# Kernel optimization log

Measured on AMD Instinct MI355X. Metric: run time of the kernel, lower is better.

Reference implementation:

```python
import jax, jax.numpy as jnp
import numpy as np

HEADS = 8
DIM_HEAD = 32
TOP_K = 256
KMEANS_ITERS = 10
EPS_LN = 1e-6
EPS_L2 = 1e-12


def chan_layer_norm(x, gamma, beta):
    # x: (b, c, L); normalize across channel dim (biased variance)
    mean = jnp.mean(x, axis=1, keepdims=True)
    var = jnp.var(x, axis=1, keepdims=True)
    return gamma * (x - mean) / (jnp.sqrt(var) + EPS_LN) + beta


def l2norm_ch(t):
    # F.normalize(t, dim=1): L2-normalize over channel axis of (B, c, L)
    n = jnp.linalg.norm(t, axis=1, keepdims=True)
    return t / jnp.maximum(n, EPS_L2)


def conv1x1(x, w):
    # x: (b, c_in, L), w: (c_out, c_in)  -> (b, c_out, L)
    return jnp.einsum('oc,bcl->bol', w, x)


def _dist2(x, c):
    # squared L2 distances, x: (N, d), c: (k, d) -> (N, k)
    return (jnp.sum(x * x, -1, keepdims=True)
            - 2.0 * x @ c.T
            + jnp.sum(c * c, -1)[None, :])


def kmeans_fit(x, k, iters):
    # Lloyd's algorithm, deterministic init = first k points
    c0 = x[:k]

    def step(c, _):
        assign = jnp.argmin(_dist2(x, c), axis=-1)           # (N,)
        sums = jax.ops.segment_sum(x, assign, num_segments=k)
        cnts = jax.ops.segment_sum(jnp.ones((x.shape[0],), x.dtype), assign,
                                   num_segments=k)
        new_c = jnp.where(cnts[:, None] > 0,
                          sums / jnp.maximum(cnts, 1.0)[:, None], c)
        return new_c, None

    c, _ = jax.lax.scan(step, c0, None, length=iters)
    return c


def select_best_ind(q, k, v, top_k):
    # q: (B, Lq, d), k/v: (B, Lk, d); B = b*heads
    B, Lk, d = k.shape
    q_flat = q.reshape(-1, d)
    centroids = kmeans_fit(q_flat, top_k, KMEANS_ITERS)       # (top_k, d)
    k_flat = k.reshape(-1, d)
    k_cluster = jnp.argmin(_dist2(k_flat, centroids), axis=-1).reshape(B, Lk)
    k_centers = centroids[k_cluster]                          # (B, Lk, d)
    k_dist = jnp.sum(jnp.abs(k_centers - k), axis=-1)         # (B, Lk)
    _, best_k = jax.lax.top_k(k_dist, top_k)                  # largest dists
    idx = best_k[:, :, None]
    k_sel = jnp.take_along_axis(k, idx, axis=1)
    v_sel = jnp.take_along_axis(v, idx, axis=1)
    return k_sel, v_sel


def reference(query_source, context, w_q, w_kv, w_out,
              ln_ctx_gamma, ln_ctx_beta, ln_q_gamma, ln_q_beta,
              ln_out_gamma, ln_out_beta, gamma_scale):
    b, c, L_query = query_source.shape
    ctx = chan_layer_norm(context, ln_ctx_gamma, ln_ctx_beta)
    qs = chan_layer_norm(query_source, ln_q_gamma, ln_q_beta)

    kv = conv1x1(ctx, w_kv)                                   # (b, 2*inner, Lc)
    k, v = jnp.split(kv, 2, axis=1)
    q = conv1x1(qs, w_q)                                      # (b, inner, Lq)

    def fold(t):  # b (h c) L -> (b h) c L
        B, hc, L = t.shape
        return t.reshape(B, HEADS, DIM_HEAD, L).reshape(B * HEADS, DIM_HEAD, L)

    q, k, v = fold(q), fold(k), fold(v)
    q, k = l2norm_ch(q), l2norm_ch(k)
    # b d L -> b L d
    q = jnp.swapaxes(q, 1, 2)
    k = jnp.swapaxes(k, 1, 2)
    v = jnp.swapaxes(v, 1, 2)

    k, v = select_best_ind(q, k, v, TOP_K)

    sim = jnp.einsum('bid,bjd->bij', q, k)                    # (b*h, Lq, top_k)
    attn = jax.nn.softmax(sim, axis=-1)
    out = jnp.einsum('bij,bjd->bid', attn, v)                 # (b*h, Lq, dh)

    out = out.reshape(b, HEADS, L_query, DIM_HEAD)
    out = jnp.transpose(out, (0, 1, 3, 2)).reshape(b, HEADS * DIM_HEAD, L_query)
    out = conv1x1(out, w_out)
    out = chan_layer_norm(out, ln_out_gamma, ln_out_beta)
    return gamma_scale[0] * out + query_source


def setup_inputs() -> dict:
    key = jax.random.key(0)
    ks = jax.random.split(key, 8)
    dim, inner = 256, HEADS * DIM_HEAD
    b, Lq, Lc = 2, 4096, 4096
    inp = {
        'query_source': jax.random.normal(ks[0], (b, dim, Lq), jnp.float32),
        'context': jax.random.normal(ks[1], (b, dim, Lc), jnp.float32),
        'w_q': jax.random.normal(ks[2], (inner, dim), jnp.float32) * 0.05,
        'w_kv': jax.random.normal(ks[3], (2 * inner, dim), jnp.float32) * 0.05,
        'w_out': jax.random.normal(ks[4], (dim, inner), jnp.float32) * 0.05,
        'ln_ctx_gamma': jnp.ones((1, dim, 1), jnp.float32),
        'ln_ctx_beta': jnp.zeros((1, dim, 1), jnp.float32),
        'ln_q_gamma': jnp.ones((1, dim, 1), jnp.float32),
        'ln_q_beta': jnp.zeros((1, dim, 1), jnp.float32),
        'ln_out_gamma': jnp.ones((1, dim, 1), jnp.float32),
        'ln_out_beta': jnp.zeros((1, dim, 1), jnp.float32),
        'gamma_scale': jax.random.normal(ks[5], (1,), jnp.float32),
    }
    return inp
```

## Files before the change

### kernel.cpp

```cpp
#include <hip/hip_runtime.h>
#include <math.h>

#define CDIM 256
#define LSEQ 4096
#define NBH 16
#define NPTS 65536
#define KC 256

__device__ __forceinline__ float fadd(float a, float b){ return __fadd_rn(a,b); }
__device__ __forceinline__ float fmul(float a, float b){ return __fmul_rn(a,b); }
__device__ __forceinline__ float fsub(float a, float b){ return __fsub_rn(a,b); }

__device__ __forceinline__ float sum32_np(const float* e){
    float l[16];
    #pragma unroll
    for (int j = 0; j < 16; j++) l[j] = fadd(e[j], e[j + 16]);
    float t3[8];
    #pragma unroll
    for (int j = 0; j < 8; j++) t3[j] = fadd(l[j], l[j + 8]);
    float t6[4];
    #pragma unroll
    for (int j = 0; j < 4; j++) t6[j] = fadd(t3[j], t3[j + 4]);
    return fadd(fadd(t6[0], t6[2]), fadd(t6[1], t6[3]));
}

__global__ __launch_bounds__(64) void ln2_np(
        const float* __restrict__ x0, const float* __restrict__ g0,
        const float* __restrict__ bt0, float* __restrict__ y0,
        const float* __restrict__ x1, const float* __restrict__ g1,
        const float* __restrict__ bt1, float* __restrict__ y1) {
    int gid = blockIdx.x * 64 + threadIdx.x;
    int which = gid >> 13;
    int r = gid & 8191;
    int b = r >> 12, l = r & 4095;
    const float* x  = which ? x1 : x0;
    const float* g  = which ? g1 : g0;
    const float* bt = which ? bt1 : bt0;
    float* y        = which ? y1 : y0;
    const float* xb = x + (size_t)b * CDIM * LSEQ + l;
    float s = 0.f;
    #pragma unroll 8
    for (int c = 0; c < 256; c++) s = fadd(s, xb[(size_t)c * LSEQ]);
    float mean = __fdiv_rn(s, 256.f);
    float s2 = 0.f;
    #pragma unroll 8
    for (int c = 0; c < 256; c++) {
        float d = fsub(xb[(size_t)c * LSEQ], mean);
        s2 = fadd(s2, fmul(d, d));
    }
    float var = __fdiv_rn(s2, 256.f);
    float den = fadd(__fsqrt_rn(var), 1e-6f);
    float* yb = y + (size_t)b * CDIM * LSEQ + l;
    #pragma unroll 4
    for (int c = 0; c < 256; c++) {
        float d = fsub(xb[(size_t)c * LSEQ], mean);
        yb[(size_t)c * LSEQ] = fadd(__fdiv_rn(fmul(g[c], d), den), bt[c]);
    }
}

__global__ __launch_bounds__(256) void conv_all(
        const float* __restrict__ Wkv, const float* __restrict__ Xkv,
        float* __restrict__ Ykv,
        const float* __restrict__ Wq, const float* __restrict__ Xq,
        float* __restrict__ Yq) {
    __shared__ float ws[8 * 256];
    int tid = threadIdx.x;
    int l0 = blockIdx.x * 512 + tid * 2;
    bool qpath = blockIdx.y >= 64;
    int yb = qpath ? (blockIdx.y - 64) : blockIdx.y;
    int o0 = yb * 8;
    int b = blockIdx.z;
    const float* W = qpath ? Wq : Wkv;
    const float* X = qpath ? Xq : Xkv;
    {
        const float4* wb4 = (const float4*)(W + (size_t)o0 * CDIM);
        float4* ws4s = (float4*)ws;
        for (int i = tid; i < 8 * 64; i += 256) ws4s[i] = wb4[i];
    }
    __syncthreads();
    const float* xb = X + (size_t)b * CDIM * LSEQ;
    float acc[8][2];
    #pragma unroll
    for (int oo = 0; oo < 8; oo++) { acc[oo][0] = 0.f; acc[oo][1] = 0.f; }
    const float4* ws4 = (const float4*)ws;
    bool sop = qpath || (blockIdx.y < 32);
    if (sop) {
        for (int c = 0; c < 256; c += 4) {
            float2 x0q = *(const float2*)(xb + (size_t)(c + 0) * LSEQ + l0);
            float2 x1q = *(const float2*)(xb + (size_t)(c + 1) * LSEQ + l0);
            float2 x2q = *(const float2*)(xb + (size_t)(c + 2) * LSEQ + l0);
            float2 x3q = *(const float2*)(xb + (size_t)(c + 3) * LSEQ + l0);
            #pragma unroll
            for (int oo = 0; oo < 8; oo++) {
                float4 w = ws4[(oo * 256 + c) >> 2];
                acc[oo][0] = fadd(acc[oo][0], fmul(w.x, x0q.x));
                acc[oo][0] = fadd(acc[oo][0], fmul(w.y, x1q.x));
                acc[oo][0] = fadd(acc[oo][0], fmul(w.z, x2q.x));
                acc[oo][0] = fadd(acc[oo][0], fmul(w.w, x3q.x));
                acc[oo][1] = fadd(acc[oo][1], fmul(w.x, x0q.y));
                acc[oo][1] = fadd(acc[oo][1], fmul(w.y, x1q.y));
                acc[oo][1] = fadd(acc[oo][1], fmul(w.z, x2q.y));
                acc[oo][1] = fadd(acc[oo][1], fmul(w.w, x3q.y));
            }
        }
    } else {
        for (int c = 0; c < 256; c += 4) {
            float2 x0q = *(const float2*)(xb + (size_t)(c + 0) * LSEQ + l0);
            float2 x1q = *(const float2*)(xb + (size_t)(c + 1) * LSEQ + l0);
            float2 x2q = *(const float2*)(xb + (size_t)(c + 2) * LSEQ + l0);
            float2 x3q = *(const float2*)(xb + (size_t)(c + 3) * LSEQ + l0);
            #pragma unroll
            for (int oo = 0; oo < 8; oo++) {
                float4 w = ws4[(oo * 256 + c) >> 2];
                acc[oo][0] = __builtin_fmaf(w.x, x0q.x, acc[oo][0]);
                acc[oo][0] = __builtin_fmaf(w.y, x1q.x, acc[oo][0]);
                acc[oo][0] = __builtin_fmaf(w.z, x2q.x, acc[oo][0]);
                acc[oo][0] = __builtin_fmaf(w.w, x3q.x, acc[oo][0]);
                acc[oo][1] = __builtin_fmaf(w.x, x0q.y, acc[oo][1]);
                acc[oo][1] = __builtin_fmaf(w.y, x1q.y, acc[oo][1]);
                acc[oo][1] = __builtin_fmaf(w.z, x2q.y, acc[oo][1]);
                acc[oo][1] = __builtin_fmaf(w.w, x3q.y, acc[oo][1]);
            }
        }
    }
    float* Y = qpath ? Yq : Ykv;
    int rows = qpath ? 256 : 512;
    #pragma unroll
    for (int oo = 0; oo < 8; oo++)
        *(float2*)(Y + ((size_t)b * rows + o0 + oo) * LSEQ + l0) =
            make_float2(acc[oo][0], acc[oo][1]);
}

template<bool EXACT>
__global__ __launch_bounds__(256) void conv_q8(const float* __restrict__ W,
        const float* __restrict__ X, float* __restrict__ Y) {
    __shared__ float ws[8 * 256];
    int tid = threadIdx.x;
    int l0 = blockIdx.x * 512 + tid * 2;
    int o0 = blockIdx.y * 8;
    int b = blockIdx.z;
    {
        const float4* wb4 = (const float4*)(W + (size_t)o0 * CDIM);
        float4* ws4s = (float4*)ws;
        for (int i = tid; i < 8 * 64; i += 256) ws4s[i] = wb4[i];
    }
    __syncthreads();
    const float* xb = X + (size_t)b * CDIM * LSEQ;
    float acc[8][2];
    #pragma unroll
    for (int oo = 0; oo < 8; oo++) { acc[oo][0] = 0.f; acc[oo][1] = 0.f; }
    const float4* ws4 = (const float4*)ws;
    for (int c = 0; c < 256; c += 4) {
        float2 x0q = *(const float2*)(xb + (size_t)(c + 0) * LSEQ + l0);
        float2 x1q = *(const float2*)(xb + (size_t)(c + 1) * LSEQ + l0);
        float2 x2q = *(const float2*)(xb + (size_t)(c + 2) * LSEQ + l0);
        float2 x3q = *(const float2*)(xb + (size_t)(c + 3) * LSEQ + l0);
        #pragma unroll
        for (int oo = 0; oo < 8; oo++) {
            float4 w = ws4[(oo * 256 + c) >> 2];
            if (EXACT) {
                acc[oo][0] = fadd(acc[oo][0], fmul(w.x, x0q.x));
                acc[oo][0] = fadd(acc[oo][0], fmul(w.y, x1q.x));
                acc[oo][0] = fadd(acc[oo][0], fmul(w.z, x2q.x));
                acc[oo][0] = fadd(acc[oo][0], fmul(w.w, x3q.x));
                acc[oo][1] = fadd(acc[oo][1], fmul(w.x, x0q.y));
                acc[oo][1] = fadd(acc[oo][1], fmul(w.y, x1q.y));
                acc[oo][1] = fadd(acc[oo][1], fmul(w.z, x2q.y));
                acc[oo][1] = fadd(acc[oo][1], fmul(w.w, x3q.y));
            } else {
                acc[oo][0] = __builtin_fmaf(w.x, x0q.x, acc[oo][0]);
                acc[oo][0] = __builtin_fmaf(w.y, x1q.x, acc[oo][0]);
                acc[oo][0] = __builtin_fmaf(w.z, x2q.x, acc[oo][0]);
                acc[oo][0] = __builtin_fmaf(w.w, x3q.x, acc[oo][0]);
                acc[oo][1] = __builtin_fmaf(w.x, x0q.y, acc[oo][1]);
                acc[oo][1] = __builtin_fmaf(w.y, x1q.y, acc[oo][1]);
                acc[oo][1] = __builtin_fmaf(w.z, x2q.y, acc[oo][1]);
                acc[oo][1] = __builtin_fmaf(w.w, x3q.y, acc[oo][1]);
            }
        }
    }
    #pragma unroll
    for (int oo = 0; oo < 8; oo++)
        *(float2*)(Y + ((size_t)b * 256 + o0 + oo) * LSEQ + l0) =
            make_float2(acc[oo][0], acc[oo][1]);
}

__device__ __forceinline__ void fold_body(const float* __restrict__ src,
        int srcRows, int row0, int donorm, float* __restrict__ dst,
        float* __restrict__ xxout, float* __restrict__ centout,
        float* __restrict__ ccout, int p) {
    int bh = p >> 12, l = p & 4095;
    int b = bh >> 3, h = bh & 7;
    const float* sp = src + ((size_t)b * srcRows + row0 + h * 32) * LSEQ + l;
    float x[32];
    #pragma unroll
    for (int t = 0; t < 32; t++) x[t] = sp[(size_t)t * LSEQ];
    float4* dp4 = (float4*)(dst + (size_t)p * 32);
    if (donorm) {
        float ss = 0.f;
        #pragma unroll
        for (int t = 0; t < 32; t++) ss = fadd(ss, fmul(x[t], x[t]));
        float n = __fsqrt_rn(ss);
        float den = fmaxf(n, 1e-12f);
        #pragma unroll
        for (int t = 0; t < 32; t++) x[t] = __fdiv_rn(x[t], den);
    }
    #pragma unroll
    for (int t = 0; t < 8; t++)
        dp4[t] = make_float4(x[4*t], x[4*t+1], x[4*t+2], x[4*t+3]);
    if (xxout) {
        float e[32];
        #pragma unroll
        for (int t = 0; t < 32; t++) e[t] = fmul(x[t], x[t]);
        float xv = sum32_np(e);
        xxout[p] = xv;
        if (centout && p < KC) {
            float4* cp4 = (float4*)(centout + (size_t)p * 32);
            #pragma unroll
            for (int t = 0; t < 8; t++)
                cp4[t] = make_float4(x[4*t], x[4*t+1], x[4*t+2], x[4*t+3]);
            ccout[p] = xv;
        }
    }
}

__global__ __launch_bounds__(256) void fold3_np(const float* __restrict__ kvbuf,
        const float* __restrict__ qbuf, float* __restrict__ k_t,
        float* __restrict__ v_t, float* __restrict__ q_t,
        float* __restrict__ xx, float* __restrict__ cent, float* __restrict__ cc) {
    int blk = blockIdx.x, tid = threadIdx.x;
    if (blk < 256) {
        fold_body(kvbuf, 512, 0, 1, k_t, nullptr, nullptr, nullptr, blk * 256 + tid);
    } else if (blk < 512) {
        fold_body(kvbuf, 512, 256, 0, v_t, nullptr, nullptr, nullptr, (blk - 256) * 256 + tid);
    } else {
        fold_body(qbuf, 256, 0, 1, q_t, xx, cent, cc, (blk - 512) * 256 + tid);
    }
}

__global__ __launch_bounds__(512, 2) void assign4p(const float* __restrict__ pts,
        const float* __restrict__ xx, const float* __restrict__ cent,
        const float* __restrict__ cc, int* __restrict__ asn, int* __restrict__ hist) {
    __shared__ float sc[8192];
    __shared__ float scc[256];
    __shared__ int bins[256];
    int tid = threadIdx.x, c = blockIdx.x;
    {
        const float4* c4 = (const float4*)cent;
        float4* s4 = (float4*)sc;
        for (int i = tid; i < 2048; i += 512) s4[i] = c4[i];
    }
    if (tid < 256) { scc[tid] = cc[tid]; bins[tid] = 0; }
    __syncthreads();
    int pg = tid >> 3, slice = tid & 7;
    int pb = c * 256 + pg * 4;
    float x[4][32];
    float xp[4];
    #pragma unroll
    for (int i = 0; i < 4; i++) {
        const float4* pp = (const float4*)(pts + (size_t)(pb + i) * 32);
        #pragma unroll
        for (int t = 0; t < 8; t++) {
            float4 f = pp[t];
            x[i][4*t] = f.x; x[i][4*t+1] = f.y; x[i][4*t+2] = f.z; x[i][4*t+3] = f.w;
        }
        xp[i] = xx[pb + i];
    }
    float bd[4] = {3.4e38f, 3.4e38f, 3.4e38f, 3.4e38f};
    int bj[4] = {0, 0, 0, 0};
    int jbase = slice * 32;
    for (int jj = 0; jj < 32; jj++) {
        int j = jbase + jj;
        const float4* cj = (const float4*)(sc + j * 32);
        float w[32];
        #pragma unroll
        for (int t = 0; t < 8; t++) {
            float4 f = cj[t];
            w[4*t] = f.x; w[4*t+1] = f.y; w[4*t+2] = f.z; w[4*t+3] = f.w;
        }
        float sj = scc[j];
        #pragma unroll
        for (int i = 0; i < 4; i++) {
            float g = 0.f;
            #pragma unroll
            for (int t = 0; t < 32; t++) g = __builtin_fmaf(x[i][t], w[t], g);
            float d = fadd(fsub(xp[i], fmul(2.f, g)), sj);
            if (d < bd[i]) { bd[i] = d; bj[i] = j; }
        }
    }
    #pragma unroll
    for (int i = 0; i < 4; i++) {
        float ob; int oj;
        ob = __shfl_xor(bd[i], 1); oj = __shfl_xor(bj[i], 1);
        if (ob < bd[i]) { bd[i] = ob; bj[i] = oj; }
        ob = __shfl_xor(bd[i], 2); oj = __shfl_xor(bj[i], 2);
        if (ob < bd[i]) { bd[i] = ob; bj[i] = oj; }
        ob = __shfl_xor(bd[i], 4); oj = __shfl_xor(bj[i], 4);
        if (ob < bd[i]) { bd[i] = ob; bj[i] = oj; }
    }
    if (slice == 0) {
        #pragma unroll
        for (int i = 0; i < 4; i++) {
            asn[pb + i] = bj[i];
            atomicAdd(&bins[bj[i]], 1);
        }
    }
    __syncthreads();
    if (tid < 256) hist[c * 256 + tid] = bins[tid];
}

__global__ __launch_bounds__(256) void scan_chunks(const int* __restrict__ hist,
        int* __restrict__ chunkbase, int* __restrict__ totals) {
    __shared__ int a[256];
    int j = blockIdx.x, c = threadIdx.x;
    a[c] = hist[(size_t)c * 256 + j];
    __syncthreads();
    for (int d = 1; d < 256; d <<= 1) {
        int v = a[c];
        int u = (c >= d) ? a[c - d] : 0;
        __syncthreads();
        a[c] = v + u;
        __syncthreads();
    }
    chunkbase[(size_t)c * 256 + j] = (c == 0) ? 0 : a[c - 1];
    if (c == 255) totals[j] = a[255];
}

__global__ __launch_bounds__(256) void scatter_v5(const int* __restrict__ asn,
        const int* __restrict__ chunkbase, const int* __restrict__ totals,
        int* __restrict__ perm) {
    __shared__ int cb[256];
    __shared__ int al[256];
    int c = blockIdx.x, tid = threadIdx.x;
    cb[tid] = totals[tid];
    al[tid] = asn[c * 256 + tid];
    __syncthreads();
    for (int d = 1; d < 256; d <<= 1) {
        int v = cb[tid];
        int u = (tid >= d) ? cb[tid - d] : 0;
        __syncthreads();
        cb[tid] = v + u;
        __syncthreads();
    }
    int my = al[tid];
    int base = (my == 0) ? 0 : cb[my - 1];
    int r = 0;
    for (int i = 0; i < tid; i++) r += (al[i] == my) ? 1 : 0;
    perm[base + chunkbase[(size_t)c * 256 + my] + r] = c * 256 + tid;
}

#define STILE 128
__global__ __launch_bounds__(256) void sumk_v4(const float* __restrict__ pts,
        const int* __restrict__ perm, const int* __restrict__ totals,
        float* __restrict__ cent, float* __restrict__ cc) {
    __shared__ int cb[256];
    __shared__ float buf[2][STILE][32];
    int j = blockIdx.x, tid = threadIdx.x;
    cb[tid] = totals[tid];
    __syncthreads();
    for (int d = 1; d < 256; d <<= 1) {
        int v = cb[tid];
        int u = (tid >= d) ? cb[tid - d] : 0;
        __syncthreads();
        cb[tid] = v + u;
        __syncthreads();
    }
    int base = (j == 0) ? 0 : cb[j - 1];
    int n = totals[j];
    int t = tid & 31, r0 = tid >> 5;
    for (int r = r0; r < STILE; r += 8) {
        if (r < n) buf[0][r][t] = pts[(size_t)perm[base + r] * 32 + t];
    }
    __syncthreads();
    float s = 0.f;
    int b = 0;
    for (int i0 = 0; i0 < n; i0 += STILE, b ^= 1) {
        int nx = i0 + STILE;
        if (nx < n) {
            for (int r = r0; r < STILE; r += 8) {
                int g = nx + r;
                if (g < n) buf[b ^ 1][r][t] = pts[(size_t)perm[base + g] * 32 + t];
            }
        }
        if (tid < 32) {
            int m = n - i0; if (m > STILE) m = STILE;
            int i = 0;
            for (; i + 4 <= m; i += 4) {
                s = fadd(s, buf[b][i][tid]);
                s = fadd(s, buf[b][i + 1][tid]);
                s = fadd(s, buf[b][i + 2][tid]);
                s = fadd(s, buf[b][i + 3][tid]);
            }
            for (; i < m; i++) s = fadd(s, buf[b][i][tid]);
        }
        __syncthreads();
    }
    if (tid < 32) {
        float v;
        if (n > 0) {
            v = __fdiv_rn(s, (float)n);
            cent[(size_t)j * 32 + tid] = v;
        } else {
            v = cent[(size_t)j * 32 + tid];
        }
        float e = fmul(v, v);
        e = fadd(e, __shfl_xor(e, 16));
        e = fadd(e, __shfl_xor(e, 8));
        e = fadd(e, __shfl_xor(e, 4));
        e = fadd(e, __shfl_xor(e, 2));
        e = fadd(e, __shfl_xor(e, 1));
        if (tid == 0) cc[j] = e;
    }
}

__global__ __launch_bounds__(512, 2) void kdist4p(const float* __restrict__ pts,
        const float* __restrict__ cent, const float* __restrict__ cc,
        float* __restrict__ kd) {
    __shared__ float sc[8192];
    __shared__ float scc[256];
    int tid = threadIdx.x, c = blockIdx.x;
    {
        const float4* c4 = (const float4*)cent;
        float4* s4 = (float4*)sc;
        for (int i = tid; i < 2048; i += 512) s4[i] = c4[i];
    }
    if (tid < 256) scc[tid] = cc[tid];
    __syncthreads();
    int pg = tid >> 3, slice = tid & 7;
    int pb = c * 256 + pg * 4;
    float x[4][32];
    float xp[4];
    #pragma unroll
    for (int i = 0; i < 4; i++) {
        const float4* pp = (const float4*)(pts + (size_t)(pb + i) * 32);
        #pragma unroll
        for (int t = 0; t < 8; t++) {
            float4 f = pp[t];
            x[i][4*t] = f.x; x[i][4*t+1] = f.y; x[i][4*t+2] = f.z; x[i][4*t+3] = f.w;
        }
        float e[32];
        #pragma unroll
        for (int t = 0; t < 32; t++) e[t] = fmul(x[i][t], x[i][t]);
        xp[i] = sum32_np(e);
    }
    float bd[4] = {3.4e38f, 3.4e38f, 3.4e38f, 3.4e38f};
    int bj[4] = {0, 0, 0, 0};
    int jbase = slice * 32;
    for (int jj = 0; jj < 32; jj++) {
        int j = jbase + jj;
        const float4* cj = (const float4*)(sc + j * 32);
        float w[32];
        #pragma unroll
        for (int t = 0; t < 8; t++) {
            float4 f = cj[t];
            w[4*t] = f.x; w[4*t+1] = f.y; w[4*t+2] = f.z; w[4*t+3] = f.w;
        }
        float sj = scc[j];
        #pragma unroll
        for (int i = 0; i < 4; i++) {
            float g = 0.f;
            #pragma unroll
            for (int t = 0; t < 32; t++) g = __builtin_fmaf(x[i][t], w[t], g);
            float d = fadd(fsub(xp[i], fmul(2.f, g)), sj);
            if (d < bd[i]) { bd[i] = d; bj[i] = j; }
        }
    }
    #pragma unroll
    for (int i = 0; i < 4; i++) {
        float ob; int oj;
        ob = __shfl_xor(bd[i], 1); oj = __shfl_xor(bj[i], 1);
        if (ob < bd[i]) { bd[i] = ob; bj[i] = oj; }
        ob = __shfl_xor(bd[i], 2); oj = __shfl_xor(bj[i], 2);
        if (ob < bd[i]) { bd[i] = ob; bj[i] = oj; }
        ob = __shfl_xor(bd[i], 4); oj = __shfl_xor(bj[i], 4);
        if (ob < bd[i]) { bd[i] = ob; bj[i] = oj; }
    }
    if (slice == 0) {
        #pragma unroll
        for (int i = 0; i < 4; i++) {
            const float* cb = &sc[bj[i] * 32];
            float e[32];
            #pragma unroll
            for (int t = 0; t < 32; t++) e[t] = fabsf(fsub(cb[t], x[i][t]));
            kd[pb + i] = sum32_np(e);
        }
    }
}

__global__ __launch_bounds__(256) void topk_v3(const float* __restrict__ kd,
        const float* __restrict__ k_t, const float* __restrict__ v_t,
        float* __restrict__ ksel, float* __restrict__ vsel) {
    __shared__ int wsum[4];
    __shared__ int sc1[256];
    __shared__ int out_src[256];
    int bh = blockIdx.x, tid = threadIdx.x;
    int wave = tid >> 6, lane = tid & 63;
    unsigned uv[16];
    {
        const unsigned* kdu = (const unsigned*)(kd + (size_t)bh * 4096);
        #pragma unroll
        for (int q = 0; q < 16; q++) uv[q] = kdu[tid * 16 + q];
    }
    unsigned T = 0u;
    for (int bit = 31; bit >= 0; bit--) {
        unsigned cand = T | (1u << bit);
        int c = 0;
        #pragma unroll
        for (int q = 0; q < 16; q++) c += (uv[q] >= cand) ? 1 : 0;
        c += __shfl_xor(c, 32); c += __shfl_xor(c, 16); c += __shfl_xor(c, 8);
        c += __shfl_xor(c, 4);  c += __shfl_xor(c, 2);  c += __shfl_xor(c, 1);
        if (lane == 0) wsum[wave] = c;
        __syncthreads();
        int tot = wsum[0] + wsum[1] + wsum[2] + wsum[3];
        __syncthreads();
        if (tot >= 256) T = cand;
    }
    int r;
    {
        int c = 0;
        #pragma unroll
        for (int q = 0; q < 16; q++) c += (uv[q] > T) ? 1 : 0;
        c += __shfl_xor(c, 32); c += __shfl_xor(c, 16); c += __shfl_xor(c, 8);
        c += __shfl_xor(c, 4);  c += __shfl_xor(c, 2);  c += __shfl_xor(c, 1);
        if (lane == 0) wsum[wave] = c;
        __syncthreads();
        r = 256 - (wsum[0] + wsum[1] + wsum[2] + wsum[3]);
        __syncthreads();
    }
    int ec = 0;
    #pragma unroll
    for (int q = 0; q < 16; q++) ec += (uv[q] == T) ? 1 : 0;
    sc1[tid] = ec;
    __syncthreads();
    for (int d = 1; d < 256; d <<= 1) {
        int t0 = sc1[tid];
        int u0 = (tid >= d) ? sc1[tid - d] : 0;
        __syncthreads();
        sc1[tid] = t0 + u0;
        __syncthreads();
    }
    int erank = (tid == 0) ? 0 : sc1[tid - 1];
    __syncthreads();
    bool incl[16];
    int ic = 0;
    #pragma unroll
    for (int q = 0; q < 16; q++) {
        unsigned u = uv[q];
        bool inc;
        if (u > T) inc = true;
        else if (u == T) { inc = (erank < r); erank++; }
        else inc = false;
        incl[q] = inc;
        ic += inc ? 1 : 0;
    }
    sc1[tid] = ic;
    __syncthreads();
    for (int d = 1; d < 256; d <<= 1) {
        int t0 = sc1[tid];
        int u0 = (tid >= d) ? sc1[tid - d] : 0;
        __syncthreads();
        sc1[tid] = t0 + u0;
        __syncthreads();
    }
    int pos = (tid == 0) ? 0 : sc1[tid - 1];
    int base_i = tid * 16;
    #pragma unroll
    for (int q = 0; q < 16; q++) {
        if (incl[q]) out_src[pos++] = base_i + q;
    }
    __syncthreads();
    for (int e = tid; e < 256 * 32; e += 256) {
        int jj = e >> 5, t = e & 31;
        int src = out_src[jj];
        ksel[(size_t)bh * 8192 + e] = k_t[((size_t)bh * 4096 + src) * 32 + t];
        vsel[(size_t)bh * 8192 + e] = v_t[((size_t)bh * 4096 + src) * 32 + t];
    }
}

#define HP4 2052
__global__ __launch_bounds__(256, 2) void attn_v4(const float* __restrict__ q_t,
        const float* __restrict__ ksel, const float* __restrict__ vsel,
        float* __restrict__ out) {
    __shared__ float sk[4 * HP4];
    __shared__ float sv[4 * HP4];
    int bh = blockIdx.y, tid = threadIdx.x;
    {
        const float4* gk = (const float4*)(ksel + (size_t)bh * 8192);
        const float4* gv = (const float4*)(vsel + (size_t)bh * 8192);
        for (int i = tid; i < 2048; i += 256) {
            int s = i >> 9, idx = i & 511;
            ((float4*)(sk + s * HP4))[idx] = gk[i];
            ((float4*)(sv + s * HP4))[idx] = gv[i];
        }
    }
    __syncthreads();
    int grp = tid >> 3;
    int dh = tid & 1;
    int slice = (tid >> 1) & 3;
    int p0 = bh * 4096 + blockIdx.x * 128 + grp * 4;
    float q[4][16];
    #pragma unroll
    for (int i = 0; i < 4; i++) {
        const float4* qp = (const float4*)(q_t + (size_t)(p0 + i) * 32 + dh * 16);
        #pragma unroll
        for (int t = 0; t < 4; t++) {
            float4 f = qp[t];
            q[i][4*t] = f.x; q[i][4*t+1] = f.y; q[i][4*t+2] = f.z; q[i][4*t+3] = f.w;
        }
    }
    float o[4][16];
    #pragma unroll
    for (int i = 0; i < 4; i++)
        #pragma unroll
        for (int t = 0; t < 16; t++) o[i][t] = 0.f;
    float ls[4] = {0.f, 0.f, 0.f, 0.f};
    const float* kb = sk + slice * HP4 + dh * 16;
    const float* vb = sv + slice * HP4 + dh * 16;
    for (int j = 0; j < 64; j++) {
        float kf[16];
        #pragma unroll
        for (int t = 0; t < 4; t++) {
            float4 f = *(const float4*)(kb + j * 32 + t * 4);
            kf[4*t] = f.x; kf[4*t+1] = f.y; kf[4*t+2] = f.z; kf[4*t+3] = f.w;
        }
        float ps[4];
        #pragma unroll
        for (int i = 0; i < 4; i++) {
            float a = 0.f, b2 = 0.f, c2 = 0.f, d2 = 0.f;
            #pragma unroll
            for (int t = 0; t < 4; t++) {
                a  += q[i][4*t]   * kf[4*t];
                b2 += q[i][4*t+1] * kf[4*t+1];
                c2 += q[i][4*t+2] * kf[4*t+2];
                d2 += q[i][4*t+3] * kf[4*t+3];
            }
            ps[i] = (a + b2) + (c2 + d2);
        }
        #pragma unroll
        for (int i = 0; i < 4; i++) ps[i] += __shfl_xor(ps[i], 1);
        float w[4];
        #pragma unroll
        for (int i = 0; i < 4; i++) {
            w[i] = __expf(ps[i] - 1.0f);
            ls[i] += w[i];
        }
        float vf[16];
        #pragma unroll
        for (int t = 0; t < 4; t++) {
            float4 f = *(const float4*)(vb + j * 32 + t * 4);
            vf[4*t] = f.x; vf[4*t+1] = f.y; vf[4*t+2] = f.z; vf[4*t+3] = f.w;
        }
        #pragma unroll
        for (int i = 0; i < 4; i++)
            #pragma unroll
            for (int t = 0; t < 16; t++) o[i][t] += w[i] * vf[t];
    }
    #pragma unroll
    for (int i = 0; i < 4; i++) {
        #pragma unroll
        for (int t = 0; t < 16; t++) {
            o[i][t] += __shfl_xor(o[i][t], 2);
            o[i][t] += __shfl_xor(o[i][t], 4);
        }
        ls[i] += __shfl_xor(ls[i], 2);
        ls[i] += __shfl_xor(ls[i], 4);
    }
    if (slice == 0) {
        #pragma unroll
        for (int i = 0; i < 4; i++) {
            float inv = 1.f / ls[i];
            float4* op = (float4*)(out + (size_t)(p0 + i) * 32 + dh * 16);
            #pragma unroll
            for (int t = 0; t < 4; t++)
                op[t] = make_float4(o[i][4*t]*inv, o[i][4*t+1]*inv,
                                    o[i][4*t+2]*inv, o[i][4*t+3]*inv);
        }
    }
}

__global__ __launch_bounds__(256) void unfold_kernel(const float* __restrict__ att,
        float* __restrict__ Fo) {
    __shared__ float tbuf[32][65];
    int bh = blockIdx.y, l0 = blockIdx.x * 64;
    int b = bh >> 3, h = bh & 7;
    int tid = threadIdx.x;
    #pragma unroll
    for (int r = 0; r < 8; r++) {
        int e = r * 256 + tid;
        int l = e >> 5, d = e & 31;
        tbuf[d][l] = att[((size_t)bh * 4096 + l0 + l) * 32 + d];
    }
    __syncthreads();
    #pragma unroll
    for (int r = 0; r < 8; r++) {
        int e = r * 256 + tid;
        int d = e >> 6, l = e & 63;
        Fo[((size_t)b * 256 + h * 32 + d) * LSEQ + l0 + l] = tbuf[d][l];
    }
}

__global__ __launch_bounds__(64) void lnres_np(const float* __restrict__ x,
        const float* __restrict__ g, const float* __restrict__ bt,
        const float* __restrict__ gs, const float* __restrict__ qsrc,
        float* __restrict__ y) {
    int gid = blockIdx.x * 64 + threadIdx.x;
    int b = gid >> 12, l = gid & 4095;
    const float* xb = x + (size_t)b * CDIM * LSEQ + l;
    float s = 0.f;
    #pragma unroll 8
    for (int c = 0; c < 256; c++) s = fadd(s, xb[(size_t)c * LSEQ]);
    float mean = __fdiv_rn(s, 256.f);
    float s2 = 0.f;
    #pragma unroll 8
    for (int c = 0; c < 256; c++) {
        float d = fsub(xb[(size_t)c * LSEQ], mean);
        s2 = fadd(s2, fmul(d, d));
    }
    float var = __fdiv_rn(s2, 256.f);
    float den = fadd(__fsqrt_rn(var), 1e-6f);
    float scale = gs[0];
    const float* qb = qsrc + (size_t)b * CDIM * LSEQ + l;
    float* yb = y + (size_t)b * CDIM * LSEQ + l;
    #pragma unroll 4
    for (int c = 0; c < 256; c++) {
        float d = fsub(xb[(size_t)c * LSEQ], mean);
        float r = fadd(__fdiv_rn(fmul(g[c], d), den), bt[c]);
        yb[(size_t)c * LSEQ] = fadd(fmul(scale, r), qb[(size_t)c * LSEQ]);
    }
}

extern "C" void kernel_launch(void* const* d_in, const int* in_sizes, int n_in,
                              void* d_out, int out_size, void* d_ws, size_t ws_size,
                              hipStream_t stream) {
    const float* qsrc   = (const float*)d_in[0];
    const float* ctx    = (const float*)d_in[1];
    const float* w_q    = (const float*)d_in[2];
    const float* w_kv   = (const float*)d_in[3];
    const float* w_out  = (const float*)d_in[4];
    const float* g_ctx  = (const float*)d_in[5];
    const float* b_ctx  = (const float*)d_in[6];
    const float* g_q    = (const float*)d_in[7];
    const float* b_q    = (const float*)d_in[8];
    const float* g_out  = (const float*)d_in[9];
    const float* b_out  = (const float*)d_in[10];
    const float* gs     = (const float*)d_in[11];

    char* base = (char*)d_ws;
    const size_t MB = 1024 * 1024;
    float* yln   = (float*)base;
    float* att   = (float*)base;
    float* kvbuf = (float*)(base + 8 * MB);
    float* y32   = (float*)(base + 8 * MB);
    float* qbuf  = (float*)(base + 24 * MB);
    float* Fo    = (float*)(base + 24 * MB);
    float* q_t   = (float*)(base + 32 * MB);
    float* k_t   = (float*)(base + 40 * MB);
    float* v_t   = (float*)(base + 48 * MB);
    char* SM = base + 56 * MB;
    float* xx_q      = (float*)(SM + 0);
    float* cent      = (float*)(SM + 512 * 1024);
    float* cc        = (float*)(SM + 576 * 1024);
    int*   totals    = (int*)  (SM + 640 * 1024);
    int*   asn       = (int*)  (SM + 704 * 1024);
    int*   hist      = (int*)  (SM + 960 * 1024);
    int*   chunkbase = (int*)  (SM + 1472 * 1024);
    int*   perm      = (int*)  (SM + 1984 * 1024);
    float* kd        = (float*)(SM + 2240 * 1024);
    float* ksel      = (float*)(SM + 2496 * 1024);
    float* vsel      = (float*)(SM + 3008 * 1024);
    float* yln_q     = (float*)(base + 60 * MB);

    ln2_np<<<256, 64, 0, stream>>>(ctx, g_ctx, b_ctx, yln,
                                   qsrc, g_q, b_q, yln_q);
    conv_all<<<dim3(8, 96, 2), 256, 0, stream>>>(w_kv, yln, kvbuf,
                                                 w_q, yln_q, qbuf);
    fold3_np<<<768, 256, 0, stream>>>(kvbuf, qbuf, k_t, v_t, q_t, xx_q, cent, cc);

    for (int it = 0; it < 10; it++) {
        assign4p<<<256, 512, 0, stream>>>(q_t, xx_q, cent, cc, asn, hist);
        scan_chunks<<<256, 256, 0, stream>>>(hist, chunkbase, totals);
        scatter_v5<<<256, 256, 0, stream>>>(asn, chunkbase, totals, perm);
        sumk_v4<<<256, 256, 0, stream>>>(q_t, perm, totals, cent, cc);
    }

    kdist4p<<<256, 512, 0, stream>>>(k_t, cent, cc, kd);
    topk_v3<<<16, 256, 0, stream>>>(kd, k_t, v_t, ksel, vsel);
    attn_v4<<<dim3(32, 16), 256, 0, stream>>>(q_t, ksel, vsel, att);
    unfold_kernel<<<dim3(64, 16), 256, 0, stream>>>(att, Fo);
    conv_q8<false><<<dim3(8, 32, 2), 256, 0, stream>>>(w_out, Fo, y32);
    lnres_np<<<128, 64, 0, stream>>>(y32, g_out, b_out, gs, qsrc, (float*)d_out);
}
```

Measured before the change: 985.8 us.

## Widen conv output tile, read weights directly, repartition k-means assign work

The fused input conv now computes 16 output channels per block instead of 8, which halves the number of blocks and the re-reads of the activation tile. Both conv kernels drop the shared-memory weight staging and its barrier and read weights straight from global memory as wave-uniform loads. The assign and kdist kernels now give each thread 2 points and 64 centroids instead of 4 points and 32 centroids, cutting register pressure, and drop the two-blocks-per-CU launch bound. The trade-offs are more accumulator registers in the conv and more centroid reads per point in the distance kernels.

```diff
diff --git a/kernel.cpp b/kernel.cpp
--- a/kernel.cpp
+++ b/kernel.cpp
@@ -58,32 +58,24 @@
     }
 }
 
-__global__ __launch_bounds__(256) void conv_all(
+__global__ __launch_bounds__(256) void conv_all16(
         const float* __restrict__ Wkv, const float* __restrict__ Xkv,
         float* __restrict__ Ykv,
         const float* __restrict__ Wq, const float* __restrict__ Xq,
         float* __restrict__ Yq) {
-    __shared__ float ws[8 * 256];
     int tid = threadIdx.x;
     int l0 = blockIdx.x * 512 + tid * 2;
-    bool qpath = blockIdx.y >= 64;
-    int yb = qpath ? (blockIdx.y - 64) : blockIdx.y;
-    int o0 = yb * 8;
+    bool qpath = blockIdx.y >= 32;
+    int yb = qpath ? (blockIdx.y - 32) : blockIdx.y;
+    int o0 = yb * 16;
     int b = blockIdx.z;
-    const float* W = qpath ? Wq : Wkv;
+    const float4* w4 = (const float4*)((qpath ? Wq : Wkv) + (size_t)o0 * CDIM);
     const float* X = qpath ? Xq : Xkv;
-    {
-        const float4* wb4 = (const float4*)(W + (size_t)o0 * CDIM);
-        float4* ws4s = (float4*)ws;
-        for (int i = tid; i < 8 * 64; i += 256) ws4s[i] = wb4[i];
-    }
-    __syncthreads();
     const float* xb = X + (size_t)b * CDIM * LSEQ;
-    float acc[8][2];
-    #pragma unroll
-    for (int oo = 0; oo < 8; oo++) { acc[oo][0] = 0.f; acc[oo][1] = 0.f; }
-    const float4* ws4 = (const float4*)ws;
-    bool sop = qpath || (blockIdx.y < 32);
+    float acc[16][2];
+    #pragma unroll
+    for (int oo = 0; oo < 16; oo++) { acc[oo][0] = 0.f; acc[oo][1] = 0.f; }
+    bool sop = qpath || (blockIdx.y < 16);
     if (sop) {
         for (int c = 0; c < 256; c += 4) {
             float2 x0q = *(const float2*)(xb + (size_t)(c + 0) * LSEQ + l0);
@@ -91,8 +83,8 @@
             float2 x2q = *(const float2*)(xb + (size_t)(c + 2) * LSEQ + l0);
             float2 x3q = *(const float2*)(xb + (size_t)(c + 3) * LSEQ + l0);
             #pragma unroll
-            for (int oo = 0; oo < 8; oo++) {
-                float4 w = ws4[(oo * 256 + c) >> 2];
+            for (int oo = 0; oo < 16; oo++) {
+                float4 w = w4[(oo * 256 + c) >> 2];
                 acc[oo][0] = fadd(acc[oo][0], fmul(w.x, x0q.x));
                 acc[oo][0] = fadd(acc[oo][0], fmul(w.y, x1q.x));
                 acc[oo][0] = fadd(acc[oo][0], fmul(w.z, x2q.x));
@@ -110,8 +102,8 @@
             float2 x2q = *(const float2*)(xb + (size_t)(c + 2) * LSEQ + l0);
             float2 x3q = *(const float2*)(xb + (size_t)(c + 3) * LSEQ + l0);
             #pragma unroll
-            for (int oo = 0; oo < 8; oo++) {
-                float4 w = ws4[(oo * 256 + c) >> 2];
+            for (int oo = 0; oo < 16; oo++) {
+                float4 w = w4[(oo * 256 + c) >> 2];
                 acc[oo][0] = __builtin_fmaf(w.x, x0q.x, acc[oo][0]);
                 acc[oo][0] = __builtin_fmaf(w.y, x1q.x, acc[oo][0]);
                 acc[oo][0] = __builtin_fmaf(w.z, x2q.x, acc[oo][0]);
@@ -126,7 +118,7 @@
     float* Y = qpath ? Yq : Ykv;
     int rows = qpath ? 256 : 512;
     #pragma unroll
-    for (int oo = 0; oo < 8; oo++)
+    for (int oo = 0; oo < 16; oo++)
         *(float2*)(Y + ((size_t)b * rows + o0 + oo) * LSEQ + l0) =
             make_float2(acc[oo][0], acc[oo][1]);
 }
@@ -134,22 +126,15 @@
 template<bool EXACT>
 __global__ __launch_bounds__(256) void conv_q8(const float* __restrict__ W,
         const float* __restrict__ X, float* __restrict__ Y) {
-    __shared__ float ws[8 * 256];
     int tid = threadIdx.x;
     int l0 = blockIdx.x * 512 + tid * 2;
     int o0 = blockIdx.y * 8;
     int b = blockIdx.z;
-    {
-        const float4* wb4 = (const float4*)(W + (size_t)o0 * CDIM);
-        float4* ws4s = (float4*)ws;
-        for (int i = tid; i < 8 * 64; i += 256) ws4s[i] = wb4[i];
-    }
-    __syncthreads();
+    const float4* w4 = (const float4*)(W + (size_t)o0 * CDIM);
     const float* xb = X + (size_t)b * CDIM * LSEQ;
     float acc[8][2];
     #pragma unroll
     for (int oo = 0; oo < 8; oo++) { acc[oo][0] = 0.f; acc[oo][1] = 0.f; }
-    const float4* ws4 = (const float4*)ws;
     for (int c = 0; c < 256; c += 4) {
         float2 x0q = *(const float2*)(xb + (size_t)(c + 0) * LSEQ + l0);
         float2 x1q = *(const float2*)(xb + (size_t)(c + 1) * LSEQ + l0);
@@ -157,7 +142,7 @@
         float2 x3q = *(const float2*)(xb + (size_t)(c + 3) * LSEQ + l0);
         #pragma unroll
         for (int oo = 0; oo < 8; oo++) {
-            float4 w = ws4[(oo * 256 + c) >> 2];
+            float4 w = w4[(oo * 256 + c) >> 2];
             if (EXACT) {
                 acc[oo][0] = fadd(acc[oo][0], fmul(w.x, x0q.x));
                 acc[oo][0] = fadd(acc[oo][0], fmul(w.y, x1q.x));
@@ -238,7 +223,7 @@
     }
 }
 
-__global__ __launch_bounds__(512, 2) void assign4p(const float* __restrict__ pts,
+__global__ __launch_bounds__(512) void assign4p(const float* __restrict__ pts,
         const float* __restrict__ xx, const float* __restrict__ cent,
         const float* __restrict__ cc, int* __restrict__ asn, int* __restrict__ hist) {
     __shared__ float sc[8192];
@@ -252,12 +237,12 @@
     }
     if (tid < 256) { scc[tid] = cc[tid]; bins[tid] = 0; }
     __syncthreads();
-    int pg = tid >> 3, slice = tid & 7;
-    int pb = c * 256 + pg * 4;
-    float x[4][32];
-    float xp[4];
-    #pragma unroll
-    for (int i = 0; i < 4; i++) {
+    int pg = tid >> 2, quarter = tid & 3;
+    int pb = c * 256 + pg * 2;
+    float x[2][32];
+    float xp[2];
+    #pragma unroll
+    for (int i = 0; i < 2; i++) {
         const float4* pp = (const float4*)(pts + (size_t)(pb + i) * 32);
         #pragma unroll
         for (int t = 0; t < 8; t++) {
@@ -266,10 +251,10 @@
         }
         xp[i] = xx[pb + i];
     }
-    float bd[4] = {3.4e38f, 3.4e38f, 3.4e38f, 3.4e38f};
-    int bj[4] = {0, 0, 0, 0};
-    int jbase = slice * 32;
-    for (int jj = 0; jj < 32; jj++) {
+    float bd[2] = {3.4e38f, 3.4e38f};
+    int bj[2] = {0, 0};
+    int jbase = quarter * 64;
+    for (int jj = 0; jj < 64; jj++) {
         int j = jbase + jj;
         const float4* cj = (const float4*)(sc + j * 32);
         float w[32];
@@ -280,7 +265,7 @@
         }
         float sj = scc[j];
         #pragma unroll
-        for (int i = 0; i < 4; i++) {
+        for (int i = 0; i < 2; i++) {
             float g = 0.f;
             #pragma unroll
             for (int t = 0; t < 32; t++) g = __builtin_fmaf(x[i][t], w[t], g);
@@ -289,18 +274,16 @@
         }
     }
     #pragma unroll
-    for (int i = 0; i < 4; i++) {
+    for (int i = 0; i < 2; i++) {
         float ob; int oj;
         ob = __shfl_xor(bd[i], 1); oj = __shfl_xor(bj[i], 1);
         if (ob < bd[i]) { bd[i] = ob; bj[i] = oj; }
         ob = __shfl_xor(bd[i], 2); oj = __shfl_xor(bj[i], 2);
         if (ob < bd[i]) { bd[i] = ob; bj[i] = oj; }
-        ob = __shfl_xor(bd[i], 4); oj = __shfl_xor(bj[i], 4);
-        if (ob < bd[i]) { bd[i] = ob; bj[i] = oj; }
-    }
-    if (slice == 0) {
-        #pragma unroll
-        for (int i = 0; i < 4; i++) {
+    }
+    if (quarter == 0) {
+        #pragma unroll
+        for (int i = 0; i < 2; i++) {
             asn[pb + i] = bj[i];
             atomicAdd(&bins[bj[i]], 1);
         }
@@ -413,7 +396,7 @@
     }
 }
 
-__global__ __launch_bounds__(512, 2) void kdist4p(const float* __restrict__ pts,
+__global__ __launch_bounds__(512) void kdist4p(const float* __restrict__ pts,
         const float* __restrict__ cent, const float* __restrict__ cc,
         float* __restrict__ kd) {
     __shared__ float sc[8192];
@@ -426,12 +409,12 @@
     }
     if (tid < 256) scc[tid] = cc[tid];
     __syncthreads();
-    int pg = tid >> 3, slice = tid & 7;
-    int pb = c * 256 + pg * 4;
-    float x[4][32];
-    float xp[4];
-    #pragma unroll
-    for (int i = 0; i < 4; i++) {
+    int pg = tid >> 2, quarter = tid & 3;
+    int pb = c * 256 + pg * 2;
+    float x[2][32];
+    float xp[2];
+    #pragma unroll
+    for (int i = 0; i < 2; i++) {
         const float4* pp = (const float4*)(pts + (size_t)(pb + i) * 32);
         #pragma unroll
         for (int t = 0; t < 8; t++) {
@@ -443,10 +426,10 @@
         for (int t = 0; t < 32; t++) e[t] = fmul(x[i][t], x[i][t]);
         xp[i] = sum32_np(e);
     }
-    float bd[4] = {3.4e38f, 3.4e38f, 3.4e38f, 3.4e38f};
-    int bj[4] = {0, 0, 0, 0};
-    int jbase = slice * 32;
-    for (int jj = 0; jj < 32; jj++) {
+    float bd[2] = {3.4e38f, 3.4e38f};
+    int bj[2] = {0, 0};
+    int jbase = quarter * 64;
+    for (int jj = 0; jj < 64; jj++) {
         int j = jbase + jj;
         const float4* cj = (const float4*)(sc + j * 32);
         float w[32];
@@ -457,7 +440,7 @@
         }
         float sj = scc[j];
         #pragma unroll
-        for (int i = 0; i < 4; i++) {
+        for (int i = 0; i < 2; i++) {
             float g = 0.f;
             #pragma unroll
             for (int t = 0; t < 32; t++) g = __builtin_fmaf(x[i][t], w[t], g);
@@ -466,18 +449,16 @@
         }
     }
     #pragma unroll
-    for (int i = 0; i < 4; i++) {
+    for (int i = 0; i < 2; i++) {
         float ob; int oj;
         ob = __shfl_xor(bd[i], 1); oj = __shfl_xor(bj[i], 1);
         if (ob < bd[i]) { bd[i] = ob; bj[i] = oj; }
         ob = __shfl_xor(bd[i], 2); oj = __shfl_xor(bj[i], 2);
         if (ob < bd[i]) { bd[i] = ob; bj[i] = oj; }
-        ob = __shfl_xor(bd[i], 4); oj = __shfl_xor(bj[i], 4);
-        if (ob < bd[i]) { bd[i] = ob; bj[i] = oj; }
-    }
-    if (slice == 0) {
-        #pragma unroll
-        for (int i = 0; i < 4; i++) {
+    }
+    if (quarter == 0) {
+        #pragma unroll
+        for (int i = 0; i < 2; i++) {
             const float* cb = &sc[bj[i] * 32];
             float e[32];
             #pragma unroll
@@ -772,8 +753,8 @@
 
     ln2_np<<<256, 64, 0, stream>>>(ctx, g_ctx, b_ctx, yln,
                                    qsrc, g_q, b_q, yln_q);
-    conv_all<<<dim3(8, 96, 2), 256, 0, stream>>>(w_kv, yln, kvbuf,
-                                                 w_q, yln_q, qbuf);
+    conv_all16<<<dim3(8, 48, 2), 256, 0, stream>>>(w_kv, yln, kvbuf,
+                                                   w_q, yln_q, qbuf);
     fold3_np<<<768, 256, 0, stream>>>(kvbuf, qbuf, k_t, v_t, q_t, xx_q, cent, cc);
 
     for (int it = 0; it < 10; it++) {
```

Measured after the change: 971.1 us. Within noise of the previous version (-1.5%).
